# Optimization experiments

Measured on AMD Instinct MI355X. Metric: run time of the kernel, lower is better.

The kernel has to match this reference:

```python
import jax, jax.numpy as jnp
import numpy as np

SIZE = 512
NUM_HEADS = 8
HEAD_SIZE = SIZE // NUM_HEADS
EPS = 1e-5  # GroupNorm default eps


def setup_inputs() -> dict:
    key = jax.random.key(0)
    ks = jax.random.split(key, 8)
    B, T, D = 2, 2048, SIZE
    mk = lambda k: jax.random.normal(k, (D, D), dtype=jnp.float32) / D
    return {
        "x": jax.random.normal(ks[0], (B, T, D), dtype=jnp.float32),
        "W_Q": mk(ks[1]),
        "W_K": mk(ks[2]),
        "W_V": mk(ks[3]),
        "W_G": mk(ks[4]),
        "W_O": mk(ks[5]),
        "gn_weight": jnp.ones((D,), dtype=jnp.float32),
        "gn_bias": jnp.zeros((D,), dtype=jnp.float32),
    }


def _retention(x, W_Q, W_K, W_V):
    B, T, D = x.shape
    H, dh = NUM_HEADS, HEAD_SIZE
    # projections -> (B, H, T, dh)
    q = (x @ W_Q).reshape(B, T, H, dh).transpose(0, 2, 1, 3)
    k = (x @ W_K).reshape(B, T, H, dh).transpose(0, 2, 1, 3)
    v = (x @ W_V).reshape(B, T, H, dh).transpose(0, 2, 1, 3)
    # multi-scale per-head decay: gamma_h = 1 - 2^{-5-h}
    gammas = 1.0 - jnp.exp2(-5.0 - jnp.arange(H, dtype=jnp.float32))
    idx = jnp.arange(T)
    diff = (idx[:, None] - idx[None, :]).astype(jnp.float32)  # (T, T)
    causal = diff >= 0
    # D[h, n, m] = gamma_h^{n-m} for n >= m else 0
    decay = jnp.where(causal[None], jnp.exp(diff[None] * jnp.log(gammas)[:, None, None]), 0.0)
    scores = jnp.einsum("bhtd,bhsd->bhts", q, k) / jnp.sqrt(jnp.float32(dh))
    out = jnp.einsum("bhts,bhsd->bhtd", scores * decay[None], v)
    return out.transpose(0, 2, 1, 3).reshape(B, T, D)


def _group_norm(y, weight, bias):
    # GroupNorm(NUM_HEADS, SIZE) over flattened (B*T, SIZE)
    B, T, D = y.shape
    g = y.reshape(B * T, NUM_HEADS, HEAD_SIZE)
    mean = jnp.mean(g, axis=-1, keepdims=True)
    var = jnp.var(g, axis=-1, keepdims=True)
    g = (g - mean) / jnp.sqrt(var + EPS)
    g = g.reshape(B * T, D) * weight + bias
    return g.reshape(B, T, D)


def reference(x, W_Q, W_K, W_V, W_G, W_O, gn_weight, gn_bias):
    ret = _retention(x, W_Q, W_K, W_V)          # (B, T, D)
    normed = _group_norm(ret, gn_weight, gn_bias)  # (B, T, D)
    return jax.nn.silu(x @ W_G + normed) @ W_O
```

## Files before the change

kernel.cpp:

```cpp
#include <hip/hip_runtime.h>
#include <hip/hip_bf16.h>
#include <math.h>

#define DMODEL 512
#define T_SEQ 2048
#define NH 8
#define DH 64
#define M_ROWS 4096
#define LDST 72
#define EPST 136

typedef short s16x8 __attribute__((ext_vector_type(8)));
typedef float f32x4 __attribute__((ext_vector_type(4)));

static __device__ __forceinline__ unsigned short f2bf(float f) {
  __hip_bfloat16 h = __float2bfloat16(f);
  return *(unsigned short*)&h;
}
static __device__ __forceinline__ float bf2f(unsigned short u) {
  union { unsigned int i; float f; } x; x.i = (unsigned int)u << 16; return x.f;
}
static __device__ __forceinline__ void gld16(void* lds, const void* g) {
  __builtin_amdgcn_global_load_lds(
      (const __attribute__((address_space(1))) unsigned int*)g,
      (__attribute__((address_space(3))) unsigned int*)lds, 16, 0, 0);
}

__global__ __launch_bounds__(256) void prep_k(
    const float* __restrict__ x, unsigned short* __restrict__ Xb,
    const float* __restrict__ W0, const float* __restrict__ W1,
    const float* __restrict__ W2, const float* __restrict__ W3,
    const float* __restrict__ W4, unsigned short* __restrict__ WT)
{
  __shared__ __align__(16) unsigned short buf[64 * LDST];
  const int bid = blockIdx.x, tid = threadIdx.x;
  if (bid < 1024) {
    const size_t i = ((size_t)bid * 256 + tid) * 8;
    float4 a = *(const float4*)&x[i];
    float4 b = *(const float4*)&x[i + 4];
    s16x8 o;
    o[0]=f2bf(a.x); o[1]=f2bf(a.y); o[2]=f2bf(a.z); o[3]=f2bf(a.w);
    o[4]=f2bf(b.x); o[5]=f2bf(b.y); o[6]=f2bf(b.z); o[7]=f2bf(b.w);
    *(s16x8*)&Xb[i] = o;
    return;
  }
  const int bid2 = bid - 1024;
  const int z = bid2 >> 6, rem = bid2 & 63;
  const int n0 = (rem & 7) * 64, k0 = (rem >> 3) * 64;
  const float* W = (z==0)?W0:(z==1)?W1:(z==2)?W2:(z==3)?W3:W4;
  int rowbase;
  if (z == 0)      rowbase = n0;
  else if (z == 1) rowbase = 512 + (n0 >> 6) * 128;
  else if (z == 2) rowbase = 512 + (n0 >> 6) * 128 + 64;
  else if (z == 3) rowbase = 1536 + n0;
  else             rowbase = 2048 + n0;
  #pragma unroll
  for (int r = 0; r < 4; ++r) {
    int idx = r * 256 + tid;
    int kr = idx >> 4, nc = idx & 15;
    float4 v = *(const float4*)&W[(size_t)(k0 + kr) * DMODEL + n0 + nc * 4];
    buf[(nc*4+0) * LDST + kr] = f2bf(v.x);
    buf[(nc*4+1) * LDST + kr] = f2bf(v.y);
    buf[(nc*4+2) * LDST + kr] = f2bf(v.z);
    buf[(nc*4+3) * LDST + kr] = f2bf(v.w);
  }
  __syncthreads();
  #pragma unroll
  for (int r = 0; r < 2; ++r) {
    int idx = r * 256 + tid;
    int nr = idx >> 3, c = idx & 7;
    *(s16x8*)&WT[((size_t)(rowbase + nr)) * DMODEL + k0 + c * 8] =
        *(const s16x8*)&buf[nr * LDST + c * 8];
  }
}

__global__ __launch_bounds__(256) void proj_kv_k(
    const unsigned short* __restrict__ A, const unsigned short* __restrict__ BT,
    unsigned short* __restrict__ Qb, unsigned short* __restrict__ Kb,
    unsigned short* __restrict__ Vb, unsigned short* __restrict__ Gb,
    float* __restrict__ AT)
{
  __shared__ __align__(16) unsigned short smem[128 * EPST];
  unsigned short* As = smem;
  unsigned short* Bs = smem + 128 * 64;
  const int ng0 = blockIdx.x * 128;
  const int m0 = blockIdx.y * 128;
  const int tid = threadIdx.x;
  const int wave = tid >> 6, lane = tid & 63;
  const int wm = wave >> 1, wn = wave & 1;
  const int n = lane & 15, quad = lane >> 4;

  int srow[4], scol[4];
  #pragma unroll
  for (int r = 0; r < 4; ++r) {
    int idx = r * 256 + tid;
    srow[r] = idx >> 3;
    scol[r] = ((idx & 7) ^ (srow[r] & 7)) * 8;
  }

  f32x4 acc[4][4];
  #pragma unroll
  for (int mi = 0; mi < 4; ++mi)
    #pragma unroll
    for (int ni = 0; ni < 4; ++ni) acc[mi][ni] = (f32x4){0.f,0.f,0.f,0.f};

  for (int k0 = 0; k0 < 512; k0 += 64) {
    #pragma unroll
    for (int r = 0; r < 4; ++r) {
      int idx = r * 256 + tid;
      gld16(&As[idx * 8], &A[(size_t)(m0 + srow[r]) * DMODEL + k0 + scol[r]]);
      gld16(&Bs[idx * 8], &BT[(size_t)(ng0 + srow[r]) * DMODEL + k0 + scol[r]]);
    }
    __syncthreads();
    #pragma unroll
    for (int kk = 0; kk < 2; ++kk) {
      s16x8 af[4], bf[4];
      #pragma unroll
      for (int mi = 0; mi < 4; ++mi) {
        int R = wm*64 + mi*16 + n, cc = (kk*4 + quad) ^ (n & 7);
        af[mi] = *(const s16x8*)&As[R * 64 + cc * 8];
      }
      #pragma unroll
      for (int ni = 0; ni < 4; ++ni) {
        int R = wn*64 + ni*16 + n, cc = (kk*4 + quad) ^ (n & 7);
        bf[ni] = *(const s16x8*)&Bs[R * 64 + cc * 8];
      }
      #pragma unroll
      for (int mi = 0; mi < 4; ++mi)
        #pragma unroll
        for (int ni = 0; ni < 4; ++ni)
          acc[mi][ni] = __builtin_amdgcn_mfma_f32_16x16x32_bf16(
              af[mi], bf[ni], acc[mi][ni], 0, 0, 0);
    }
    __syncthreads();
  }

  unsigned short* Ep = smem;
  #pragma unroll
  for (int mi = 0; mi < 4; ++mi)
    #pragma unroll
    for (int ni = 0; ni < 4; ++ni)
      #pragma unroll
      for (int r = 0; r < 4; ++r)
        Ep[(wm*64 + mi*16 + quad*4 + r) * EPST + wn*64 + ni*16 + n] =
            f2bf(acc[mi][ni][r]);
  __syncthreads();

  const int bx = blockIdx.x;
  if (bx < 4 || bx >= 12) {
    unsigned short* Cz = (bx < 4) ? Qb : Gb;
    const int n0 = (bx < 4) ? ng0 : (ng0 - 1536);
    #pragma unroll
    for (int t = 0; t < 8; ++t) {
      int idx = t * 256 + tid;
      int row = idx >> 4, u = idx & 15;
      *(s16x8*)&Cz[(size_t)(m0 + row) * DMODEL + n0 + u * 8] =
          *(const s16x8*)&Ep[row * EPST + u * 8];
    }
    return;
  }

  const int h = (ng0 - 512) >> 7;
  const float lg = log2f(1.0f - exp2f(-5.0f - (float)h));
  #pragma unroll
  for (int t = 0; t < 4; ++t) {
    int idx = t * 256 + tid;
    int row = idx >> 3, u = idx & 7;
    *(s16x8*)&Kb[(size_t)(m0 + row) * DMODEL + h*DH + u * 8] =
        *(const s16x8*)&Ep[row * EPST + u * 8];
    *(s16x8*)&Vb[(size_t)(m0 + row) * DMODEL + h*DH + u * 8] =
        *(const s16x8*)&Ep[row * EPST + 64 + u * 8];
  }

  unsigned short* Kt = smem;
  unsigned short* Vt = smem + 64 * LDST;
  #pragma unroll
  for (int cc2 = 0; cc2 < 2; ++cc2) {
    __syncthreads();
    if (wm == cc2) {
      unsigned short* Tt = (wn == 0) ? Kt : Vt;
      #pragma unroll
      for (int mi = 0; mi < 4; ++mi)
        #pragma unroll
        for (int r = 0; r < 4; ++r) {
          int m = mi*16 + quad*4 + r;
          float sc = (wn == 0) ? exp2f((float)(64 - m) * lg) : 1.0f;
          #pragma unroll
          for (int ni = 0; ni < 4; ++ni)
            Tt[(ni*16 + n) * LDST + m] = f2bf(acc[mi][ni][r] * sc);
        }
    }
    __syncthreads();
    f32x4 at[4];
    #pragma unroll
    for (int j = 0; j < 4; ++j) at[j] = (f32x4){0.f,0.f,0.f,0.f};
    #pragma unroll
    for (int kk = 0; kk < 2; ++kk) {
      s16x8 a = *(const s16x8*)&Vt[(wave*16 + n) * LDST + kk*32 + quad*8];
      #pragma unroll
      for (int j = 0; j < 4; ++j) {
        s16x8 bf = *(const s16x8*)&Kt[(j*16 + n) * LDST + kk*32 + quad*8];
        at[j] = __builtin_amdgcn_mfma_f32_16x16x32_bf16(a, bf, at[j], 0, 0, 0);
      }
    }
    const int gr = m0 + cc2 * 64;
    const int bb = gr >> 11, cchunk = (gr & 2047) >> 6;
    float* Ab = AT + (((size_t)(bb * NH + h) * 32 + cchunk) << 12);
    #pragma unroll
    for (int j = 0; j < 4; ++j)
      #pragma unroll
      for (int r = 0; r < 4; ++r)
        Ab[(wave*16 + quad*4 + r) * 64 + j*16 + n] = at[j][r];
  }
}

__global__ __launch_bounds__(256) void ret_o2_k(
    const unsigned short* __restrict__ Qb, const unsigned short* __restrict__ Kb,
    const unsigned short* __restrict__ Vb, const float* __restrict__ AT,
    const unsigned short* __restrict__ Gg, const float* __restrict__ gnw,
    const float* __restrict__ gnb, unsigned short* __restrict__ Sb)
{
  __shared__ __align__(16) unsigned short Qs[64 * 64];
  __shared__ __align__(16) unsigned short Ks[64 * 64];
  __shared__ __align__(16) unsigned short Vst[64 * LDST];
  __shared__ __align__(16) unsigned short Ss[64 * LDST];
  __shared__ __align__(16) unsigned short Ps[64 * LDST];
  const int c = (int)gridDim.x - 1 - (int)blockIdx.x;
  const int h = blockIdx.y, b = blockIdx.z;
  const int bh = b * NH + h;
  const int tid = threadIdx.x;
  const int wave = tid >> 6, lane = tid & 63;
  const int n = lane & 15, quad = lane >> 4;
  const size_t base = ((size_t)b * T_SEQ + (size_t)c * 64) * DMODEL + h * DH;
  const float lg = log2f(1.0f - exp2f(-5.0f - (float)h));
  const float lg64 = 64.0f * lg;

  #pragma unroll
  for (int r = 0; r < 2; ++r) {
    int idx = r * 256 + tid;
    int row = idx >> 3, sc = ((idx & 7) ^ (row & 7)) * 8;
    gld16(&Qs[idx * 8], &Qb[base + (size_t)row * DMODEL + sc]);
    gld16(&Ks[idx * 8], &Kb[base + (size_t)row * DMODEL + sc]);
  }
  #pragma unroll
  for (int r = 0; r < 2; ++r) {
    int idx = r * 256 + tid;
    int m = idx & 63, ch = idx >> 6;
    s16x8 vv = *(const s16x8*)&Vb[base + (size_t)m * DMODEL + ch * 8];
    #pragma unroll
    for (int e = 0; e < 8; ++e)
      Vst[(ch * 8 + e) * LDST + m] = ((unsigned short*)&vv)[e];
  }

  const float* Ac = AT + (((size_t)bh * 32) << 12) + (size_t)tid * 16;
  float4 S0 = {0,0,0,0}, S1 = S0, S2 = S0, S3 = S0;
  #pragma unroll 4
  for (int cp = 0; cp < c; ++cp) {
    const float* p = Ac + ((size_t)cp << 12);
    const float w = exp2f((float)(c - 1 - cp) * lg64);
    float4 a0 = *(const float4*)(p + 0);
    float4 a1 = *(const float4*)(p + 4);
    float4 a2 = *(const float4*)(p + 8);
    float4 a3 = *(const float4*)(p + 12);
    S0.x = fmaf(w, a0.x, S0.x); S0.y = fmaf(w, a0.y, S0.y);
    S0.z = fmaf(w, a0.z, S0.z); S0.w = fmaf(w, a0.w, S0.w);
    S1.x = fmaf(w, a1.x, S1.x); S1.y = fmaf(w, a1.y, S1.y);
    S1.z = fmaf(w, a1.z, S1.z); S1.w = fmaf(w, a1.w, S1.w);
    S2.x = fmaf(w, a2.x, S2.x); S2.y = fmaf(w, a2.y, S2.y);
    S2.z = fmaf(w, a2.z, S2.z); S2.w = fmaf(w, a2.w, S2.w);
    S3.x = fmaf(w, a3.x, S3.x); S3.y = fmaf(w, a3.y, S3.y);
    S3.z = fmaf(w, a3.z, S3.z); S3.w = fmaf(w, a3.w, S3.w);
  }
  {
    const int d2 = tid >> 2, d1b = (tid & 3) * 16;
    s16x8 lo, hi;
    lo[0]=f2bf(S0.x); lo[1]=f2bf(S0.y); lo[2]=f2bf(S0.z); lo[3]=f2bf(S0.w);
    lo[4]=f2bf(S1.x); lo[5]=f2bf(S1.y); lo[6]=f2bf(S1.z); lo[7]=f2bf(S1.w);
    hi[0]=f2bf(S2.x); hi[1]=f2bf(S2.y); hi[2]=f2bf(S2.z); hi[3]=f2bf(S2.w);
    hi[4]=f2bf(S3.x); hi[5]=f2bf(S3.y); hi[6]=f2bf(S3.z); hi[7]=f2bf(S3.w);
    *(s16x8*)&Ss[d2 * LDST + d1b] = lo;
    *(s16x8*)&Ss[d2 * LDST + d1b + 8] = hi;
  }
  __syncthreads();

  f32x4 s[4], u[4];
  #pragma unroll
  for (int j = 0; j < 4; ++j) {
    s[j] = (f32x4){0.f,0.f,0.f,0.f};
    u[j] = (f32x4){0.f,0.f,0.f,0.f};
  }
  const int RA = wave*16 + n;
  #pragma unroll
  for (int kk = 0; kk < 2; ++kk) {
    s16x8 a = *(const s16x8*)&Qs[RA * 64 + (((kk*4 + quad) ^ (RA & 7)) * 8)];
    #pragma unroll
    for (int j = 0; j < 4; ++j) {
      int RB = j*16 + n;
      s16x8 bk = *(const s16x8*)&Ks[RB * 64 + (((kk*4 + quad) ^ (RB & 7)) * 8)];
      s[j] = __builtin_amdgcn_mfma_f32_16x16x32_bf16(a, bk, s[j], 0, 0, 0);
      s16x8 bs = *(const s16x8*)&Ss[RB * LDST + kk*32 + quad*8];
      u[j] = __builtin_amdgcn_mfma_f32_16x16x32_bf16(a, bs, u[j], 0, 0, 0);
    }
  }

  float rowf[4], colf[4];
  #pragma unroll
  for (int r = 0; r < 4; ++r) rowf[r] = exp2f((float)(wave*16 + quad*4 + r) * lg);
  #pragma unroll
  for (int j = 0; j < 4; ++j) colf[j] = exp2f(-(float)(j*16 + n) * lg);

  #pragma unroll
  for (int j = 0; j < 4; ++j)
    #pragma unroll
    for (int r = 0; r < 4; ++r) {
      int i = wave*16 + quad*4 + r, mcol = j*16 + n;
      float v = (mcol <= i) ? s[j][r] * 0.125f * rowf[r] * colf[j] : 0.0f;
      Ps[i * LDST + mcol] = f2bf(v);
    }
  __syncthreads();

  #pragma unroll
  for (int r = 0; r < 2; ++r) {
    int idx = r * 256 + tid;
    int row = idx >> 3, sc = ((idx & 7) ^ (row & 7)) * 8;
    gld16(&Qs[idx * 8], &Gg[base + (size_t)row * DMODEL + sc]);
  }

  f32x4 acc[4];
  #pragma unroll
  for (int j = 0; j < 4; ++j) acc[j] = (f32x4){0.f,0.f,0.f,0.f};
  #pragma unroll
  for (int kk = 0; kk < 2; ++kk) {
    s16x8 a = *(const s16x8*)&Ps[RA * LDST + kk*32 + quad*8];
    #pragma unroll
    for (int j = 0; j < 4; ++j) {
      s16x8 bf = *(const s16x8*)&Vst[(j*16 + n) * LDST + kk*32 + quad*8];
      acc[j] = __builtin_amdgcn_mfma_f32_16x16x32_bf16(a, bf, acc[j], 0, 0, 0);
    }
  }

  float ov[4][4];
  #pragma unroll
  for (int j = 0; j < 4; ++j)
    #pragma unroll
    for (int r = 0; r < 4; ++r)
      ov[j][r] = acc[j][r] + 0.125f * rowf[r] * u[j][r];

  float gw[4], gb[4];
  #pragma unroll
  for (int j = 0; j < 4; ++j) {
    gw[j] = gnw[h*DH + j*16 + n];
    gb[j] = gnb[h*DH + j*16 + n];
  }

  float normed[4][4];
  #pragma unroll
  for (int r = 0; r < 4; ++r) {
    float sum = ov[0][r] + ov[1][r] + ov[2][r] + ov[3][r];
    float sq  = ov[0][r]*ov[0][r] + ov[1][r]*ov[1][r]
              + ov[2][r]*ov[2][r] + ov[3][r]*ov[3][r];
    #pragma unroll
    for (int off = 8; off > 0; off >>= 1) {
      sum += __shfl_xor(sum, off, 64);
      sq  += __shfl_xor(sq,  off, 64);
    }
    const float mean = sum * (1.0f / 64.0f);
    float var = sq * (1.0f / 64.0f) - mean * mean;
    var = fmaxf(var, 0.0f);
    const float rstd = rsqrtf(var + 1e-5f);
    #pragma unroll
    for (int j = 0; j < 4; ++j)
      normed[j][r] = (ov[j][r] - mean) * rstd * gw[j] + gb[j];
  }

  __syncthreads();

  #pragma unroll
  for (int r = 0; r < 4; ++r) {
    const int i = wave*16 + quad*4 + r;
    #pragma unroll
    for (int j = 0; j < 4; ++j) {
      const int col = j*16 + n;
      const int gidx = i * 64 + (((col >> 3) ^ (i & 7)) * 8) + (col & 7);
      float uu = bf2f(Qs[gidx]) + normed[j][r];
      Ps[i * LDST + col] = f2bf(uu / (1.0f + expf(-uu)));
    }
  }
  __syncthreads();
  #pragma unroll
  for (int t = 0; t < 2; ++t) {
    int idx = t * 256 + tid;
    int row = idx >> 3, u8 = idx & 7;
    *(s16x8*)&Sb[base + (size_t)row * DMODEL + u8 * 8] =
        *(const s16x8*)&Ps[row * LDST + u8 * 8];
  }
}

__global__ __launch_bounds__(256) void out_gemm_k(
    const unsigned short* __restrict__ A, const unsigned short* __restrict__ BT,
    float* __restrict__ out)
{
  __shared__ __align__(16) unsigned short As[64 * 64];
  __shared__ __align__(16) unsigned short Bs[64 * 64];
  const int n0 = blockIdx.x * 64;
  const int m0 = blockIdx.y * 64;
  const int tid = threadIdx.x;
  const int wave = tid >> 6, lane = tid & 63;
  const int wm = wave >> 1, wn = wave & 1;
  const int n = lane & 15, quad = lane >> 4;

  int srow[2], scol[2];
  #pragma unroll
  for (int r = 0; r < 2; ++r) {
    int idx = r * 256 + tid;
    srow[r] = idx >> 3;
    scol[r] = ((idx & 7) ^ (srow[r] & 7)) * 8;
  }

  f32x4 acc[2][2];
  #pragma unroll
  for (int mi = 0; mi < 2; ++mi)
    #pragma unroll
    for (int ni = 0; ni < 2; ++ni) acc[mi][ni] = (f32x4){0.f,0.f,0.f,0.f};

  for (int k0 = 0; k0 < 512; k0 += 64) {
    #pragma unroll
    for (int r = 0; r < 2; ++r) {
      int idx = r * 256 + tid;
      gld16(&As[idx * 8], &A[(size_t)(m0 + srow[r]) * DMODEL + k0 + scol[r]]);
      gld16(&Bs[idx * 8], &BT[(size_t)(n0 + srow[r]) * DMODEL + k0 + scol[r]]);
    }
    __syncthreads();
    #pragma unroll
    for (int kk = 0; kk < 2; ++kk) {
      s16x8 af[2], bf[2];
      #pragma unroll
      for (int mi = 0; mi < 2; ++mi) {
        int R = wm*32 + mi*16 + n, cc = (kk*4 + quad) ^ (n & 7);
        af[mi] = *(const s16x8*)&As[R * 64 + cc * 8];
      }
      #pragma unroll
      for (int ni = 0; ni < 2; ++ni) {
        int R = wn*32 + ni*16 + n, cc = (kk*4 + quad) ^ (n & 7);
        bf[ni] = *(const s16x8*)&Bs[R * 64 + cc * 8];
      }
      #pragma unroll
      for (int mi = 0; mi < 2; ++mi)
        #pragma unroll
        for (int ni = 0; ni < 2; ++ni)
          acc[mi][ni] = __builtin_amdgcn_mfma_f32_16x16x32_bf16(
              af[mi], bf[ni], acc[mi][ni], 0, 0, 0);
    }
    __syncthreads();
  }

  #pragma unroll
  for (int mi = 0; mi < 2; ++mi)
    #pragma unroll
    for (int ni = 0; ni < 2; ++ni)
      #pragma unroll
      for (int r = 0; r < 4; ++r)
        out[(size_t)(m0 + wm*32 + mi*16 + quad*4 + r) * DMODEL +
            n0 + wn*32 + ni*16 + n] = acc[mi][ni][r];
}

extern "C" void kernel_launch(void* const* d_in, const int* in_sizes, int n_in,
                              void* d_out, int out_size, void* d_ws, size_t ws_size,
                              hipStream_t stream) {
  const float* x   = (const float*)d_in[0];
  const float* WQ  = (const float*)d_in[1];
  const float* WK  = (const float*)d_in[2];
  const float* WV  = (const float*)d_in[3];
  const float* WG  = (const float*)d_in[4];
  const float* WO  = (const float*)d_in[5];
  const float* gnw = (const float*)d_in[6];
  const float* gnb = (const float*)d_in[7];
  float* out = (float*)d_out;

  char* ws = (char*)d_ws;
  unsigned short* Xb = (unsigned short*)(ws);
  unsigned short* Qb = (unsigned short*)(ws + 4  * (1<<20));
  unsigned short* Kb = (unsigned short*)(ws + 8  * (1<<20));
  unsigned short* Vb = (unsigned short*)(ws + 12 * (1<<20));
  unsigned short* G  = (unsigned short*)(ws + 16 * (1<<20));
  float* AT  = (float*)(ws + 24 * (1<<20));
  unsigned short* Sb = (unsigned short*)(ws + 32 * (1<<20));
  unsigned short* WT = (unsigned short*)(ws + 40 * (1<<20));
  (void)ws_size;

  prep_k<<<dim3(1024 + 320), 256, 0, stream>>>(x, Xb, WQ, WK, WV, WG, WO, WT);
  proj_kv_k<<<dim3(16, M_ROWS / 128), 256, 0, stream>>>(
      Xb, WT, Qb, Kb, Vb, G, AT);
  ret_o2_k<<<dim3(T_SEQ / 64, NH, 2), 256, 0, stream>>>(
      Qb, Kb, Vb, AT, G, gnw, gnb, Sb);
  out_gemm_k<<<dim3(8, M_ROWS / 64), 256, 0, stream>>>(
      Sb, WT + 2048 * DMODEL, out);
}
```

Baseline: 122.4 us.

## Fuse four kernels into one persistent kernel with grid-wide barriers

Replaces the four separate launches (prep, projection, retention, output GEMM) with a single persistent kernel of 512 blocks. The stages are separated by software grid barriers built on atomic counters in workspace, which is reset with a memset before launch. This removes per-launch overhead and the idle gaps between kernels. In exchange it adds barrier spin cost, fixes the shared-memory size to the largest stage, and relies on all 512 blocks being co-resident (launch bounds of 2 blocks per CU), otherwise the barrier can deadlock.

```diff
diff --git a/kernel.cpp b/kernel.cpp
--- a/kernel.cpp
+++ b/kernel.cpp
@@ -9,6 +9,7 @@
 #define M_ROWS 4096
 #define LDST 72
 #define EPST 136
+#define NBLK 512u
 
 typedef short s16x8 __attribute__((ext_vector_type(8)));
 typedef float f32x4 __attribute__((ext_vector_type(4)));
@@ -26,473 +27,473 @@
       (__attribute__((address_space(3))) unsigned int*)lds, 16, 0, 0);
 }
 
-__global__ __launch_bounds__(256) void prep_k(
-    const float* __restrict__ x, unsigned short* __restrict__ Xb,
-    const float* __restrict__ W0, const float* __restrict__ W1,
-    const float* __restrict__ W2, const float* __restrict__ W3,
-    const float* __restrict__ W4, unsigned short* __restrict__ WT)
-{
-  __shared__ __align__(16) unsigned short buf[64 * LDST];
-  const int bid = blockIdx.x, tid = threadIdx.x;
-  if (bid < 1024) {
-    const size_t i = ((size_t)bid * 256 + tid) * 8;
-    float4 a = *(const float4*)&x[i];
-    float4 b = *(const float4*)&x[i + 4];
-    s16x8 o;
-    o[0]=f2bf(a.x); o[1]=f2bf(a.y); o[2]=f2bf(a.z); o[3]=f2bf(a.w);
-    o[4]=f2bf(b.x); o[5]=f2bf(b.y); o[6]=f2bf(b.z); o[7]=f2bf(b.w);
-    *(s16x8*)&Xb[i] = o;
-    return;
-  }
-  const int bid2 = bid - 1024;
-  const int z = bid2 >> 6, rem = bid2 & 63;
-  const int n0 = (rem & 7) * 64, k0 = (rem >> 3) * 64;
-  const float* W = (z==0)?W0:(z==1)?W1:(z==2)?W2:(z==3)?W3:W4;
-  int rowbase;
-  if (z == 0)      rowbase = n0;
-  else if (z == 1) rowbase = 512 + (n0 >> 6) * 128;
-  else if (z == 2) rowbase = 512 + (n0 >> 6) * 128 + 64;
-  else if (z == 3) rowbase = 1536 + n0;
-  else             rowbase = 2048 + n0;
-  #pragma unroll
-  for (int r = 0; r < 4; ++r) {
-    int idx = r * 256 + tid;
-    int kr = idx >> 4, nc = idx & 15;
-    float4 v = *(const float4*)&W[(size_t)(k0 + kr) * DMODEL + n0 + nc * 4];
-    buf[(nc*4+0) * LDST + kr] = f2bf(v.x);
-    buf[(nc*4+1) * LDST + kr] = f2bf(v.y);
-    buf[(nc*4+2) * LDST + kr] = f2bf(v.z);
-    buf[(nc*4+3) * LDST + kr] = f2bf(v.w);
+static __device__ __forceinline__ void gbar(unsigned int* cnt) {
+  __syncthreads();
+  if (threadIdx.x == 0) {
+    __threadfence();
+    __hip_atomic_fetch_add(cnt, 1u, __ATOMIC_RELEASE, __HIP_MEMORY_SCOPE_AGENT);
+    while (__hip_atomic_load(cnt, __ATOMIC_ACQUIRE, __HIP_MEMORY_SCOPE_AGENT)
+           < NBLK) {
+      __builtin_amdgcn_s_sleep(2);
+    }
   }
   __syncthreads();
-  #pragma unroll
-  for (int r = 0; r < 2; ++r) {
-    int idx = r * 256 + tid;
-    int nr = idx >> 3, c = idx & 7;
-    *(s16x8*)&WT[((size_t)(rowbase + nr)) * DMODEL + k0 + c * 8] =
-        *(const s16x8*)&buf[nr * LDST + c * 8];
+}
+
+struct MegaArgs {
+  const float* x;
+  const float* W0; const float* W1; const float* W2;
+  const float* W3; const float* W4;
+  const float* gnw; const float* gnb;
+  unsigned short* Xb; unsigned short* WT;
+  unsigned short* Qb; unsigned short* Kb; unsigned short* Vb;
+  unsigned short* G;  unsigned short* Sb;
+  float* AT; float* out;
+  unsigned int* bar;
+};
+
+__global__ __launch_bounds__(256, 2) void mega_k(MegaArgs a)
+{
+  __shared__ __align__(16) unsigned short smem[22016];
+  const int bid = blockIdx.x, tid = threadIdx.x;
+  const int wave = tid >> 6, lane = tid & 63;
+  const int n = lane & 15, quad = lane >> 4;
+
+  for (int u = bid; u < 1344; u += 512) {
+    if (u < 1024) {
+      const size_t i = ((size_t)u * 256 + tid) * 8;
+      float4 av = *(const float4*)&a.x[i];
+      float4 bv = *(const float4*)&a.x[i + 4];
+      s16x8 o;
+      o[0]=f2bf(av.x); o[1]=f2bf(av.y); o[2]=f2bf(av.z); o[3]=f2bf(av.w);
+      o[4]=f2bf(bv.x); o[5]=f2bf(bv.y); o[6]=f2bf(bv.z); o[7]=f2bf(bv.w);
+      *(s16x8*)&a.Xb[i] = o;
+    } else {
+      const int bid2 = u - 1024;
+      const int z = bid2 >> 6, rem = bid2 & 63;
+      const int n0 = (rem & 7) * 64, k0 = (rem >> 3) * 64;
+      const float* W = (z==0)?a.W0:(z==1)?a.W1:(z==2)?a.W2:(z==3)?a.W3:a.W4;
+      int rowbase;
+      if (z == 0)      rowbase = n0;
+      else if (z == 1) rowbase = 512 + (n0 >> 6) * 128;
+      else if (z == 2) rowbase = 512 + (n0 >> 6) * 128 + 64;
+      else if (z == 3) rowbase = 1536 + n0;
+      else             rowbase = 2048 + n0;
+      unsigned short* buf = smem;
+      #pragma unroll
+      for (int r = 0; r < 4; ++r) {
+        int idx = r * 256 + tid;
+        int kr = idx >> 4, nc = idx & 15;
+        float4 v = *(const float4*)&W[(size_t)(k0 + kr) * DMODEL + n0 + nc * 4];
+        buf[(nc*4+0) * LDST + kr] = f2bf(v.x);
+        buf[(nc*4+1) * LDST + kr] = f2bf(v.y);
+        buf[(nc*4+2) * LDST + kr] = f2bf(v.z);
+        buf[(nc*4+3) * LDST + kr] = f2bf(v.w);
+      }
+      __syncthreads();
+      #pragma unroll
+      for (int r = 0; r < 2; ++r) {
+        int idx = r * 256 + tid;
+        int nr = idx >> 3, c8 = idx & 7;
+        *(s16x8*)&a.WT[((size_t)(rowbase + nr)) * DMODEL + k0 + c8 * 8] =
+            *(const s16x8*)&buf[nr * LDST + c8 * 8];
+      }
+      __syncthreads();
+    }
   }
-}
-
-__global__ __launch_bounds__(256) void proj_kv_k(
-    const unsigned short* __restrict__ A, const unsigned short* __restrict__ BT,
-    unsigned short* __restrict__ Qb, unsigned short* __restrict__ Kb,
-    unsigned short* __restrict__ Vb, unsigned short* __restrict__ Gb,
-    float* __restrict__ AT)
-{
-  __shared__ __align__(16) unsigned short smem[128 * EPST];
-  unsigned short* As = smem;
-  unsigned short* Bs = smem + 128 * 64;
-  const int ng0 = blockIdx.x * 128;
-  const int m0 = blockIdx.y * 128;
-  const int tid = threadIdx.x;
-  const int wave = tid >> 6, lane = tid & 63;
-  const int wm = wave >> 1, wn = wave & 1;
-  const int n = lane & 15, quad = lane >> 4;
-
-  int srow[4], scol[4];
-  #pragma unroll
-  for (int r = 0; r < 4; ++r) {
-    int idx = r * 256 + tid;
-    srow[r] = idx >> 3;
-    scol[r] = ((idx & 7) ^ (srow[r] & 7)) * 8;
-  }
-
-  f32x4 acc[4][4];
-  #pragma unroll
-  for (int mi = 0; mi < 4; ++mi)
-    #pragma unroll
-    for (int ni = 0; ni < 4; ++ni) acc[mi][ni] = (f32x4){0.f,0.f,0.f,0.f};
-
-  for (int k0 = 0; k0 < 512; k0 += 64) {
+  gbar(&a.bar[0]);
+
+  {
+    unsigned short* As = smem;
+    unsigned short* Bs = smem + 128 * 64;
+    const int bx = bid & 15, by = bid >> 4;
+    const int ng0 = bx * 128, m0 = by * 128;
+    const int wm = wave >> 1, wn = wave & 1;
+
+    int srow[4], scol[4];
     #pragma unroll
     for (int r = 0; r < 4; ++r) {
       int idx = r * 256 + tid;
-      gld16(&As[idx * 8], &A[(size_t)(m0 + srow[r]) * DMODEL + k0 + scol[r]]);
-      gld16(&Bs[idx * 8], &BT[(size_t)(ng0 + srow[r]) * DMODEL + k0 + scol[r]]);
-    }
-    __syncthreads();
-    #pragma unroll
-    for (int kk = 0; kk < 2; ++kk) {
-      s16x8 af[4], bf[4];
-      #pragma unroll
-      for (int mi = 0; mi < 4; ++mi) {
-        int R = wm*64 + mi*16 + n, cc = (kk*4 + quad) ^ (n & 7);
-        af[mi] = *(const s16x8*)&As[R * 64 + cc * 8];
-      }
-      #pragma unroll
-      for (int ni = 0; ni < 4; ++ni) {
-        int R = wn*64 + ni*16 + n, cc = (kk*4 + quad) ^ (n & 7);
-        bf[ni] = *(const s16x8*)&Bs[R * 64 + cc * 8];
-      }
-      #pragma unroll
-      for (int mi = 0; mi < 4; ++mi)
-        #pragma unroll
-        for (int ni = 0; ni < 4; ++ni)
-          acc[mi][ni] = __builtin_amdgcn_mfma_f32_16x16x32_bf16(
-              af[mi], bf[ni], acc[mi][ni], 0, 0, 0);
-    }
-    __syncthreads();
-  }
-
-  unsigned short* Ep = smem;
-  #pragma unroll
-  for (int mi = 0; mi < 4; ++mi)
-    #pragma unroll
-    for (int ni = 0; ni < 4; ++ni)
-      #pragma unroll
-      for (int r = 0; r < 4; ++r)
-        Ep[(wm*64 + mi*16 + quad*4 + r) * EPST + wn*64 + ni*16 + n] =
-            f2bf(acc[mi][ni][r]);
-  __syncthreads();
-
-  const int bx = blockIdx.x;
-  if (bx < 4 || bx >= 12) {
-    unsigned short* Cz = (bx < 4) ? Qb : Gb;
-    const int n0 = (bx < 4) ? ng0 : (ng0 - 1536);
-    #pragma unroll
-    for (int t = 0; t < 8; ++t) {
-      int idx = t * 256 + tid;
-      int row = idx >> 4, u = idx & 15;
-      *(s16x8*)&Cz[(size_t)(m0 + row) * DMODEL + n0 + u * 8] =
-          *(const s16x8*)&Ep[row * EPST + u * 8];
-    }
-    return;
-  }
-
-  const int h = (ng0 - 512) >> 7;
-  const float lg = log2f(1.0f - exp2f(-5.0f - (float)h));
-  #pragma unroll
-  for (int t = 0; t < 4; ++t) {
-    int idx = t * 256 + tid;
-    int row = idx >> 3, u = idx & 7;
-    *(s16x8*)&Kb[(size_t)(m0 + row) * DMODEL + h*DH + u * 8] =
-        *(const s16x8*)&Ep[row * EPST + u * 8];
-    *(s16x8*)&Vb[(size_t)(m0 + row) * DMODEL + h*DH + u * 8] =
-        *(const s16x8*)&Ep[row * EPST + 64 + u * 8];
-  }
-
-  unsigned short* Kt = smem;
-  unsigned short* Vt = smem + 64 * LDST;
-  #pragma unroll
-  for (int cc2 = 0; cc2 < 2; ++cc2) {
-    __syncthreads();
-    if (wm == cc2) {
-      unsigned short* Tt = (wn == 0) ? Kt : Vt;
-      #pragma unroll
-      for (int mi = 0; mi < 4; ++mi)
-        #pragma unroll
-        for (int r = 0; r < 4; ++r) {
-          int m = mi*16 + quad*4 + r;
-          float sc = (wn == 0) ? exp2f((float)(64 - m) * lg) : 1.0f;
+      srow[r] = idx >> 3;
+      scol[r] = ((idx & 7) ^ (srow[r] & 7)) * 8;
+    }
+
+    f32x4 acc[4][4];
+    #pragma unroll
+    for (int mi = 0; mi < 4; ++mi)
+      #pragma unroll
+      for (int ni = 0; ni < 4; ++ni) acc[mi][ni] = (f32x4){0.f,0.f,0.f,0.f};
+
+    for (int k0 = 0; k0 < 512; k0 += 64) {
+      #pragma unroll
+      for (int r = 0; r < 4; ++r) {
+        int idx = r * 256 + tid;
+        gld16(&As[idx * 8], &a.Xb[(size_t)(m0 + srow[r]) * DMODEL + k0 + scol[r]]);
+        gld16(&Bs[idx * 8], &a.WT[(size_t)(ng0 + srow[r]) * DMODEL + k0 + scol[r]]);
+      }
+      __syncthreads();
+      #pragma unroll
+      for (int kk = 0; kk < 2; ++kk) {
+        s16x8 af[4], bf[4];
+        #pragma unroll
+        for (int mi = 0; mi < 4; ++mi) {
+          int R = wm*64 + mi*16 + n, cc = (kk*4 + quad) ^ (n & 7);
+          af[mi] = *(const s16x8*)&As[R * 64 + cc * 8];
+        }
+        #pragma unroll
+        for (int ni = 0; ni < 4; ++ni) {
+          int R = wn*64 + ni*16 + n, cc = (kk*4 + quad) ^ (n & 7);
+          bf[ni] = *(const s16x8*)&Bs[R * 64 + cc * 8];
+        }
+        #pragma unroll
+        for (int mi = 0; mi < 4; ++mi)
           #pragma unroll
           for (int ni = 0; ni < 4; ++ni)
-            Tt[(ni*16 + n) * LDST + m] = f2bf(acc[mi][ni][r] * sc);
-        }
-    }
+            acc[mi][ni] = __builtin_amdgcn_mfma_f32_16x16x32_bf16(
+                af[mi], bf[ni], acc[mi][ni], 0, 0, 0);
+      }
+      __syncthreads();
+    }
+
+    unsigned short* Ep = smem;
+    #pragma unroll
+    for (int mi = 0; mi < 4; ++mi)
+      #pragma unroll
+      for (int ni = 0; ni < 4; ++ni)
+        #pragma unroll
+        for (int r = 0; r < 4; ++r)
+          Ep[(wm*64 + mi*16 + quad*4 + r) * EPST + wn*64 + ni*16 + n] =
+              f2bf(acc[mi][ni][r]);
     __syncthreads();
-    f32x4 at[4];
-    #pragma unroll
-    for (int j = 0; j < 4; ++j) at[j] = (f32x4){0.f,0.f,0.f,0.f};
-    #pragma unroll
-    for (int kk = 0; kk < 2; ++kk) {
-      s16x8 a = *(const s16x8*)&Vt[(wave*16 + n) * LDST + kk*32 + quad*8];
-      #pragma unroll
-      for (int j = 0; j < 4; ++j) {
-        s16x8 bf = *(const s16x8*)&Kt[(j*16 + n) * LDST + kk*32 + quad*8];
-        at[j] = __builtin_amdgcn_mfma_f32_16x16x32_bf16(a, bf, at[j], 0, 0, 0);
-      }
-    }
-    const int gr = m0 + cc2 * 64;
-    const int bb = gr >> 11, cchunk = (gr & 2047) >> 6;
-    float* Ab = AT + (((size_t)(bb * NH + h) * 32 + cchunk) << 12);
-    #pragma unroll
-    for (int j = 0; j < 4; ++j)
-      #pragma unroll
-      for (int r = 0; r < 4; ++r)
-        Ab[(wave*16 + quad*4 + r) * 64 + j*16 + n] = at[j][r];
+
+    if (bx < 4 || bx >= 12) {
+      unsigned short* Cz = (bx < 4) ? a.Qb : a.G;
+      const int n0 = (bx < 4) ? ng0 : (ng0 - 1536);
+      #pragma unroll
+      for (int t = 0; t < 8; ++t) {
+        int idx = t * 256 + tid;
+        int row = idx >> 4, u = idx & 15;
+        *(s16x8*)&Cz[(size_t)(m0 + row) * DMODEL + n0 + u * 8] =
+            *(const s16x8*)&Ep[row * EPST + u * 8];
+      }
+    } else {
+      const int h = (ng0 - 512) >> 7;
+      const float lg = log2f(1.0f - exp2f(-5.0f - (float)h));
+      #pragma unroll
+      for (int t = 0; t < 4; ++t) {
+        int idx = t * 256 + tid;
+        int row = idx >> 3, u = idx & 7;
+        *(s16x8*)&a.Kb[(size_t)(m0 + row) * DMODEL + h*DH + u * 8] =
+            *(const s16x8*)&Ep[row * EPST + u * 8];
+        *(s16x8*)&a.Vb[(size_t)(m0 + row) * DMODEL + h*DH + u * 8] =
+            *(const s16x8*)&Ep[row * EPST + 64 + u * 8];
+      }
+      unsigned short* Kt = smem;
+      unsigned short* Vt = smem + 64 * LDST;
+      #pragma unroll
+      for (int cc2 = 0; cc2 < 2; ++cc2) {
+        __syncthreads();
+        if (wm == cc2) {
+          unsigned short* Tt = (wn == 0) ? Kt : Vt;
+          #pragma unroll
+          for (int mi = 0; mi < 4; ++mi)
+            #pragma unroll
+            for (int r = 0; r < 4; ++r) {
+              int m = mi*16 + quad*4 + r;
+              float sc = (wn == 0) ? exp2f((float)(64 - m) * lg) : 1.0f;
+              #pragma unroll
+              for (int ni = 0; ni < 4; ++ni)
+                Tt[(ni*16 + n) * LDST + m] = f2bf(acc[mi][ni][r] * sc);
+            }
+        }
+        __syncthreads();
+        f32x4 at[4];
+        #pragma unroll
+        for (int j = 0; j < 4; ++j) at[j] = (f32x4){0.f,0.f,0.f,0.f};
+        #pragma unroll
+        for (int kk = 0; kk < 2; ++kk) {
+          s16x8 av = *(const s16x8*)&Vt[(wave*16 + n) * LDST + kk*32 + quad*8];
+          #pragma unroll
+          for (int j = 0; j < 4; ++j) {
+            s16x8 bf = *(const s16x8*)&Kt[(j*16 + n) * LDST + kk*32 + quad*8];
+            at[j] = __builtin_amdgcn_mfma_f32_16x16x32_bf16(av, bf, at[j], 0, 0, 0);
+          }
+        }
+        const int gr = m0 + cc2 * 64;
+        const int bb = gr >> 11, cchunk = (gr & 2047) >> 6;
+        float* Ab = a.AT + (((size_t)(bb * NH + h) * 32 + cchunk) << 12);
+        #pragma unroll
+        for (int j = 0; j < 4; ++j)
+          #pragma unroll
+          for (int r = 0; r < 4; ++r)
+            Ab[(wave*16 + quad*4 + r) * 64 + j*16 + n] = at[j][r];
+      }
+    }
   }
-}
-
-__global__ __launch_bounds__(256) void ret_o2_k(
-    const unsigned short* __restrict__ Qb, const unsigned short* __restrict__ Kb,
-    const unsigned short* __restrict__ Vb, const float* __restrict__ AT,
-    const unsigned short* __restrict__ Gg, const float* __restrict__ gnw,
-    const float* __restrict__ gnb, unsigned short* __restrict__ Sb)
-{
-  __shared__ __align__(16) unsigned short Qs[64 * 64];
-  __shared__ __align__(16) unsigned short Ks[64 * 64];
-  __shared__ __align__(16) unsigned short Vst[64 * LDST];
-  __shared__ __align__(16) unsigned short Ss[64 * LDST];
-  __shared__ __align__(16) unsigned short Ps[64 * LDST];
-  const int c = (int)gridDim.x - 1 - (int)blockIdx.x;
-  const int h = blockIdx.y, b = blockIdx.z;
-  const int bh = b * NH + h;
-  const int tid = threadIdx.x;
-  const int wave = tid >> 6, lane = tid & 63;
-  const int n = lane & 15, quad = lane >> 4;
-  const size_t base = ((size_t)b * T_SEQ + (size_t)c * 64) * DMODEL + h * DH;
-  const float lg = log2f(1.0f - exp2f(-5.0f - (float)h));
-  const float lg64 = 64.0f * lg;
-
-  #pragma unroll
-  for (int r = 0; r < 2; ++r) {
-    int idx = r * 256 + tid;
-    int row = idx >> 3, sc = ((idx & 7) ^ (row & 7)) * 8;
-    gld16(&Qs[idx * 8], &Qb[base + (size_t)row * DMODEL + sc]);
-    gld16(&Ks[idx * 8], &Kb[base + (size_t)row * DMODEL + sc]);
-  }
-  #pragma unroll
-  for (int r = 0; r < 2; ++r) {
-    int idx = r * 256 + tid;
-    int m = idx & 63, ch = idx >> 6;
-    s16x8 vv = *(const s16x8*)&Vb[base + (size_t)m * DMODEL + ch * 8];
-    #pragma unroll
-    for (int e = 0; e < 8; ++e)
-      Vst[(ch * 8 + e) * LDST + m] = ((unsigned short*)&vv)[e];
-  }
-
-  const float* Ac = AT + (((size_t)bh * 32) << 12) + (size_t)tid * 16;
-  float4 S0 = {0,0,0,0}, S1 = S0, S2 = S0, S3 = S0;
-  #pragma unroll 4
-  for (int cp = 0; cp < c; ++cp) {
-    const float* p = Ac + ((size_t)cp << 12);
-    const float w = exp2f((float)(c - 1 - cp) * lg64);
-    float4 a0 = *(const float4*)(p + 0);
-    float4 a1 = *(const float4*)(p + 4);
-    float4 a2 = *(const float4*)(p + 8);
-    float4 a3 = *(const float4*)(p + 12);
-    S0.x = fmaf(w, a0.x, S0.x); S0.y = fmaf(w, a0.y, S0.y);
-    S0.z = fmaf(w, a0.z, S0.z); S0.w = fmaf(w, a0.w, S0.w);
-    S1.x = fmaf(w, a1.x, S1.x); S1.y = fmaf(w, a1.y, S1.y);
-    S1.z = fmaf(w, a1.z, S1.z); S1.w = fmaf(w, a1.w, S1.w);
-    S2.x = fmaf(w, a2.x, S2.x); S2.y = fmaf(w, a2.y, S2.y);
-    S2.z = fmaf(w, a2.z, S2.z); S2.w = fmaf(w, a2.w, S2.w);
-    S3.x = fmaf(w, a3.x, S3.x); S3.y = fmaf(w, a3.y, S3.y);
-    S3.z = fmaf(w, a3.z, S3.z); S3.w = fmaf(w, a3.w, S3.w);
-  }
+  gbar(&a.bar[16]);
+
   {
-    const int d2 = tid >> 2, d1b = (tid & 3) * 16;
-    s16x8 lo, hi;
-    lo[0]=f2bf(S0.x); lo[1]=f2bf(S0.y); lo[2]=f2bf(S0.z); lo[3]=f2bf(S0.w);
-    lo[4]=f2bf(S1.x); lo[5]=f2bf(S1.y); lo[6]=f2bf(S1.z); lo[7]=f2bf(S1.w);
-    hi[0]=f2bf(S2.x); hi[1]=f2bf(S2.y); hi[2]=f2bf(S2.z); hi[3]=f2bf(S2.w);
-    hi[4]=f2bf(S3.x); hi[5]=f2bf(S3.y); hi[6]=f2bf(S3.z); hi[7]=f2bf(S3.w);
-    *(s16x8*)&Ss[d2 * LDST + d1b] = lo;
-    *(s16x8*)&Ss[d2 * LDST + d1b + 8] = hi;
-  }
-  __syncthreads();
-
-  f32x4 s[4], u[4];
-  #pragma unroll
-  for (int j = 0; j < 4; ++j) {
-    s[j] = (f32x4){0.f,0.f,0.f,0.f};
-    u[j] = (f32x4){0.f,0.f,0.f,0.f};
-  }
-  const int RA = wave*16 + n;
-  #pragma unroll
-  for (int kk = 0; kk < 2; ++kk) {
-    s16x8 a = *(const s16x8*)&Qs[RA * 64 + (((kk*4 + quad) ^ (RA & 7)) * 8)];
-    #pragma unroll
-    for (int j = 0; j < 4; ++j) {
-      int RB = j*16 + n;
-      s16x8 bk = *(const s16x8*)&Ks[RB * 64 + (((kk*4 + quad) ^ (RB & 7)) * 8)];
-      s[j] = __builtin_amdgcn_mfma_f32_16x16x32_bf16(a, bk, s[j], 0, 0, 0);
-      s16x8 bs = *(const s16x8*)&Ss[RB * LDST + kk*32 + quad*8];
-      u[j] = __builtin_amdgcn_mfma_f32_16x16x32_bf16(a, bs, u[j], 0, 0, 0);
-    }
-  }
-
-  float rowf[4], colf[4];
-  #pragma unroll
-  for (int r = 0; r < 4; ++r) rowf[r] = exp2f((float)(wave*16 + quad*4 + r) * lg);
-  #pragma unroll
-  for (int j = 0; j < 4; ++j) colf[j] = exp2f(-(float)(j*16 + n) * lg);
-
-  #pragma unroll
-  for (int j = 0; j < 4; ++j)
-    #pragma unroll
-    for (int r = 0; r < 4; ++r) {
-      int i = wave*16 + quad*4 + r, mcol = j*16 + n;
-      float v = (mcol <= i) ? s[j][r] * 0.125f * rowf[r] * colf[j] : 0.0f;
-      Ps[i * LDST + mcol] = f2bf(v);
-    }
-  __syncthreads();
-
-  #pragma unroll
-  for (int r = 0; r < 2; ++r) {
-    int idx = r * 256 + tid;
-    int row = idx >> 3, sc = ((idx & 7) ^ (row & 7)) * 8;
-    gld16(&Qs[idx * 8], &Gg[base + (size_t)row * DMODEL + sc]);
-  }
-
-  f32x4 acc[4];
-  #pragma unroll
-  for (int j = 0; j < 4; ++j) acc[j] = (f32x4){0.f,0.f,0.f,0.f};
-  #pragma unroll
-  for (int kk = 0; kk < 2; ++kk) {
-    s16x8 a = *(const s16x8*)&Ps[RA * LDST + kk*32 + quad*8];
-    #pragma unroll
-    for (int j = 0; j < 4; ++j) {
-      s16x8 bf = *(const s16x8*)&Vst[(j*16 + n) * LDST + kk*32 + quad*8];
-      acc[j] = __builtin_amdgcn_mfma_f32_16x16x32_bf16(a, bf, acc[j], 0, 0, 0);
-    }
-  }
-
-  float ov[4][4];
-  #pragma unroll
-  for (int j = 0; j < 4; ++j)
-    #pragma unroll
-    for (int r = 0; r < 4; ++r)
-      ov[j][r] = acc[j][r] + 0.125f * rowf[r] * u[j][r];
-
-  float gw[4], gb[4];
-  #pragma unroll
-  for (int j = 0; j < 4; ++j) {
-    gw[j] = gnw[h*DH + j*16 + n];
-    gb[j] = gnb[h*DH + j*16 + n];
-  }
-
-  float normed[4][4];
-  #pragma unroll
-  for (int r = 0; r < 4; ++r) {
-    float sum = ov[0][r] + ov[1][r] + ov[2][r] + ov[3][r];
-    float sq  = ov[0][r]*ov[0][r] + ov[1][r]*ov[1][r]
-              + ov[2][r]*ov[2][r] + ov[3][r]*ov[3][r];
-    #pragma unroll
-    for (int off = 8; off > 0; off >>= 1) {
-      sum += __shfl_xor(sum, off, 64);
-      sq  += __shfl_xor(sq,  off, 64);
-    }
-    const float mean = sum * (1.0f / 64.0f);
-    float var = sq * (1.0f / 64.0f) - mean * mean;
-    var = fmaxf(var, 0.0f);
-    const float rstd = rsqrtf(var + 1e-5f);
-    #pragma unroll
-    for (int j = 0; j < 4; ++j)
-      normed[j][r] = (ov[j][r] - mean) * rstd * gw[j] + gb[j];
-  }
-
-  __syncthreads();
-
-  #pragma unroll
-  for (int r = 0; r < 4; ++r) {
-    const int i = wave*16 + quad*4 + r;
-    #pragma unroll
-    for (int j = 0; j < 4; ++j) {
-      const int col = j*16 + n;
-      const int gidx = i * 64 + (((col >> 3) ^ (i & 7)) * 8) + (col & 7);
-      float uu = bf2f(Qs[gidx]) + normed[j][r];
-      Ps[i * LDST + col] = f2bf(uu / (1.0f + expf(-uu)));
-    }
-  }
-  __syncthreads();
-  #pragma unroll
-  for (int t = 0; t < 2; ++t) {
-    int idx = t * 256 + tid;
-    int row = idx >> 3, u8 = idx & 7;
-    *(s16x8*)&Sb[base + (size_t)row * DMODEL + u8 * 8] =
-        *(const s16x8*)&Ps[row * LDST + u8 * 8];
-  }
-}
-
-__global__ __launch_bounds__(256) void out_gemm_k(
-    const unsigned short* __restrict__ A, const unsigned short* __restrict__ BT,
-    float* __restrict__ out)
-{
-  __shared__ __align__(16) unsigned short As[64 * 64];
-  __shared__ __align__(16) unsigned short Bs[64 * 64];
-  const int n0 = blockIdx.x * 64;
-  const int m0 = blockIdx.y * 64;
-  const int tid = threadIdx.x;
-  const int wave = tid >> 6, lane = tid & 63;
-  const int wm = wave >> 1, wn = wave & 1;
-  const int n = lane & 15, quad = lane >> 4;
-
-  int srow[2], scol[2];
-  #pragma unroll
-  for (int r = 0; r < 2; ++r) {
-    int idx = r * 256 + tid;
-    srow[r] = idx >> 3;
-    scol[r] = ((idx & 7) ^ (srow[r] & 7)) * 8;
-  }
-
-  f32x4 acc[2][2];
-  #pragma unroll
-  for (int mi = 0; mi < 2; ++mi)
-    #pragma unroll
-    for (int ni = 0; ni < 2; ++ni) acc[mi][ni] = (f32x4){0.f,0.f,0.f,0.f};
-
-  for (int k0 = 0; k0 < 512; k0 += 64) {
+    unsigned short* Qs  = smem;
+    unsigned short* Ks  = smem + 4096;
+    unsigned short* Vst = smem + 8192;
+    unsigned short* Ss  = smem + 8192 + 4608;
+    unsigned short* Ps  = smem + 8192 + 9216;
+    const int c = bid & 31, h = (bid >> 5) & 7, b = bid >> 8;
+    const int bh = b * NH + h;
+    const size_t base = ((size_t)b * T_SEQ + (size_t)c * 64) * DMODEL + h * DH;
+    const float lg = log2f(1.0f - exp2f(-5.0f - (float)h));
+    const float lg64 = 64.0f * lg;
+
     #pragma unroll
     for (int r = 0; r < 2; ++r) {
       int idx = r * 256 + tid;
-      gld16(&As[idx * 8], &A[(size_t)(m0 + srow[r]) * DMODEL + k0 + scol[r]]);
-      gld16(&Bs[idx * 8], &BT[(size_t)(n0 + srow[r]) * DMODEL + k0 + scol[r]]);
+      int row = idx >> 3, sc = ((idx & 7) ^ (row & 7)) * 8;
+      gld16(&Qs[idx * 8], &a.Qb[base + (size_t)row * DMODEL + sc]);
+      gld16(&Ks[idx * 8], &a.Kb[base + (size_t)row * DMODEL + sc]);
+    }
+    #pragma unroll
+    for (int r = 0; r < 2; ++r) {
+      int idx = r * 256 + tid;
+      int m = idx & 63, ch = idx >> 6;
+      s16x8 vv = *(const s16x8*)&a.Vb[base + (size_t)m * DMODEL + ch * 8];
+      #pragma unroll
+      for (int e = 0; e < 8; ++e)
+        Vst[(ch * 8 + e) * LDST + m] = ((unsigned short*)&vv)[e];
+    }
+
+    const float* Ac = a.AT + (((size_t)bh * 32) << 12) + (size_t)tid * 16;
+    float4 S0 = {0,0,0,0}, S1 = S0, S2 = S0, S3 = S0;
+    #pragma unroll 4
+    for (int cp = 0; cp < c; ++cp) {
+      const float* p = Ac + ((size_t)cp << 12);
+      const float w = exp2f((float)(c - 1 - cp) * lg64);
+      float4 a0 = *(const float4*)(p + 0);
+      float4 a1 = *(const float4*)(p + 4);
+      float4 a2 = *(const float4*)(p + 8);
+      float4 a3 = *(const float4*)(p + 12);
+      S0.x = fmaf(w, a0.x, S0.x); S0.y = fmaf(w, a0.y, S0.y);
+      S0.z = fmaf(w, a0.z, S0.z); S0.w = fmaf(w, a0.w, S0.w);
+      S1.x = fmaf(w, a1.x, S1.x); S1.y = fmaf(w, a1.y, S1.y);
+      S1.z = fmaf(w, a1.z, S1.z); S1.w = fmaf(w, a1.w, S1.w);
+      S2.x = fmaf(w, a2.x, S2.x); S2.y = fmaf(w, a2.y, S2.y);
+      S2.z = fmaf(w, a2.z, S2.z); S2.w = fmaf(w, a2.w, S2.w);
+      S3.x = fmaf(w, a3.x, S3.x); S3.y = fmaf(w, a3.y, S3.y);
+      S3.z = fmaf(w, a3.z, S3.z); S3.w = fmaf(w, a3.w, S3.w);
+    }
+    {
+      const int d2 = tid >> 2, d1b = (tid & 3) * 16;
+      s16x8 lo, hi;
+      lo[0]=f2bf(S0.x); lo[1]=f2bf(S0.y); lo[2]=f2bf(S0.z); lo[3]=f2bf(S0.w);
+      lo[4]=f2bf(S1.x); lo[5]=f2bf(S1.y); lo[6]=f2bf(S1.z); lo[7]=f2bf(S1.w);
+      hi[0]=f2bf(S2.x); hi[1]=f2bf(S2.y); hi[2]=f2bf(S2.z); hi[3]=f2bf(S2.w);
+      hi[4]=f2bf(S3.x); hi[5]=f2bf(S3.y); hi[6]=f2bf(S3.z); hi[7]=f2bf(S3.w);
+      *(s16x8*)&Ss[d2 * LDST + d1b] = lo;
+      *(s16x8*)&Ss[d2 * LDST + d1b + 8] = hi;
     }
     __syncthreads();
+
+    f32x4 s[4], u[4];
+    #pragma unroll
+    for (int j = 0; j < 4; ++j) {
+      s[j] = (f32x4){0.f,0.f,0.f,0.f};
+      u[j] = (f32x4){0.f,0.f,0.f,0.f};
+    }
+    const int RA = wave*16 + n;
     #pragma unroll
     for (int kk = 0; kk < 2; ++kk) {
-      s16x8 af[2], bf[2];
-      #pragma unroll
-      for (int mi = 0; mi < 2; ++mi) {
-        int R = wm*32 + mi*16 + n, cc = (kk*4 + quad) ^ (n & 7);
-        af[mi] = *(const s16x8*)&As[R * 64 + cc * 8];
-      }
-      #pragma unroll
-      for (int ni = 0; ni < 2; ++ni) {
-        int R = wn*32 + ni*16 + n, cc = (kk*4 + quad) ^ (n & 7);
-        bf[ni] = *(const s16x8*)&Bs[R * 64 + cc * 8];
-      }
-      #pragma unroll
-      for (int mi = 0; mi < 2; ++mi)
-        #pragma unroll
-        for (int ni = 0; ni < 2; ++ni)
-          acc[mi][ni] = __builtin_amdgcn_mfma_f32_16x16x32_bf16(
-              af[mi], bf[ni], acc[mi][ni], 0, 0, 0);
-    }
+      s16x8 av = *(const s16x8*)&Qs[RA * 64 + (((kk*4 + quad) ^ (RA & 7)) * 8)];
+      #pragma unroll
+      for (int j = 0; j < 4; ++j) {
+        int RB = j*16 + n;
+        s16x8 bk = *(const s16x8*)&Ks[RB * 64 + (((kk*4 + quad) ^ (RB & 7)) * 8)];
+        s[j] = __builtin_amdgcn_mfma_f32_16x16x32_bf16(av, bk, s[j], 0, 0, 0);
+        s16x8 bs = *(const s16x8*)&Ss[RB * LDST + kk*32 + quad*8];
+        u[j] = __builtin_amdgcn_mfma_f32_16x16x32_bf16(av, bs, u[j], 0, 0, 0);
+      }
+    }
+
+    float rowf[4], colf[4];
+    #pragma unroll
+    for (int r = 0; r < 4; ++r) rowf[r] = exp2f((float)(wave*16 + quad*4 + r) * lg);
+    #pragma unroll
+    for (int j = 0; j < 4; ++j) colf[j] = exp2f(-(float)(j*16 + n) * lg);
+
+    #pragma unroll
+    for (int j = 0; j < 4; ++j)
+      #pragma unroll
+      for (int r = 0; r < 4; ++r) {
+        int i = wave*16 + quad*4 + r, mcol = j*16 + n;
+        float v = (mcol <= i) ? s[j][r] * 0.125f * rowf[r] * colf[j] : 0.0f;
+        Ps[i * LDST + mcol] = f2bf(v);
+      }
     __syncthreads();
+
+    #pragma unroll
+    for (int r = 0; r < 2; ++r) {
+      int idx = r * 256 + tid;
+      int row = idx >> 3, sc = ((idx & 7) ^ (row & 7)) * 8;
+      gld16(&Qs[idx * 8], &a.G[base + (size_t)row * DMODEL + sc]);
+    }
+
+    f32x4 acc[4];
+    #pragma unroll
+    for (int j = 0; j < 4; ++j) acc[j] = (f32x4){0.f,0.f,0.f,0.f};
+    #pragma unroll
+    for (int kk = 0; kk < 2; ++kk) {
+      s16x8 av = *(const s16x8*)&Ps[RA * LDST + kk*32 + quad*8];
+      #pragma unroll
+      for (int j = 0; j < 4; ++j) {
+        s16x8 bf = *(const s16x8*)&Vst[(j*16 + n) * LDST + kk*32 + quad*8];
+        acc[j] = __builtin_amdgcn_mfma_f32_16x16x32_bf16(av, bf, acc[j], 0, 0, 0);
+      }
+    }
+
+    float ov[4][4];
+    #pragma unroll
+    for (int j = 0; j < 4; ++j)
+      #pragma unroll
+      for (int r = 0; r < 4; ++r)
+        ov[j][r] = acc[j][r] + 0.125f * rowf[r] * u[j][r];
+
+    float gw[4], gb[4];
+    #pragma unroll
+    for (int j = 0; j < 4; ++j) {
+      gw[j] = a.gnw[h*DH + j*16 + n];
+      gb[j] = a.gnb[h*DH + j*16 + n];
+    }
+
+    float normed[4][4];
+    #pragma unroll
+    for (int r = 0; r < 4; ++r) {
+      float sum = ov[0][r] + ov[1][r] + ov[2][r] + ov[3][r];
+      float sq  = ov[0][r]*ov[0][r] + ov[1][r]*ov[1][r]
+                + ov[2][r]*ov[2][r] + ov[3][r]*ov[3][r];
+      #pragma unroll
+      for (int off = 8; off > 0; off >>= 1) {
+        sum += __shfl_xor(sum, off, 64);
+        sq  += __shfl_xor(sq,  off, 64);
+      }
+      const float mean = sum * (1.0f / 64.0f);
+      float var = sq * (1.0f / 64.0f) - mean * mean;
+      var = fmaxf(var, 0.0f);
+      const float rstd = rsqrtf(var + 1e-5f);
+      #pragma unroll
+      for (int j = 0; j < 4; ++j)
+        normed[j][r] = (ov[j][r] - mean) * rstd * gw[j] + gb[j];
+    }
+
+    __syncthreads();
+
+    #pragma unroll
+    for (int r = 0; r < 4; ++r) {
+      const int i = wave*16 + quad*4 + r;
+      #pragma unroll
+      for (int j = 0; j < 4; ++j) {
+        const int col = j*16 + n;
+        const int gidx = i * 64 + (((col >> 3) ^ (i & 7)) * 8) + (col & 7);
+        float uu = bf2f(Qs[gidx]) + normed[j][r];
+        Ps[i * LDST + col] = f2bf(uu / (1.0f + expf(-uu)));
+      }
+    }
+    __syncthreads();
+    #pragma unroll
+    for (int t = 0; t < 2; ++t) {
+      int idx = t * 256 + tid;
+      int row = idx >> 3, u8 = idx & 7;
+      *(s16x8*)&a.Sb[base + (size_t)row * DMODEL + u8 * 8] =
+          *(const s16x8*)&Ps[row * LDST + u8 * 8];
+    }
   }
-
-  #pragma unroll
-  for (int mi = 0; mi < 2; ++mi)
-    #pragma unroll
-    for (int ni = 0; ni < 2; ++ni)
-      #pragma unroll
-      for (int r = 0; r < 4; ++r)
-        out[(size_t)(m0 + wm*32 + mi*16 + quad*4 + r) * DMODEL +
-            n0 + wn*32 + ni*16 + n] = acc[mi][ni][r];
+  gbar(&a.bar[32]);
+
+  {
+    unsigned short* As = smem;
+    unsigned short* Bs = smem + 4096;
+    const unsigned short* BT = a.WT + 2048 * DMODEL;
+    const int n0 = (bid & 7) * 64, m0 = (bid >> 3) * 64;
+    const int wm = wave >> 1, wn = wave & 1;
+
+    int srow[2], scol[2];
+    #pragma unroll
+    for (int r = 0; r < 2; ++r) {
+      int idx = r * 256 + tid;
+      srow[r] = idx >> 3;
+      scol[r] = ((idx & 7) ^ (srow[r] & 7)) * 8;
+    }
+
+    f32x4 acc[2][2];
+    #pragma unroll
+    for (int mi = 0; mi < 2; ++mi)
+      #pragma unroll
+      for (int ni = 0; ni < 2; ++ni) acc[mi][ni] = (f32x4){0.f,0.f,0.f,0.f};
+
+    for (int k0 = 0; k0 < 512; k0 += 64) {
+      #pragma unroll
+      for (int r = 0; r < 2; ++r) {
+        int idx = r * 256 + tid;
+        gld16(&As[idx * 8], &a.Sb[(size_t)(m0 + srow[r]) * DMODEL + k0 + scol[r]]);
+        gld16(&Bs[idx * 8], &BT[(size_t)(n0 + srow[r]) * DMODEL + k0 + scol[r]]);
+      }
+      __syncthreads();
+      #pragma unroll
+      for (int kk = 0; kk < 2; ++kk) {
+        s16x8 af[2], bf[2];
+        #pragma unroll
+        for (int mi = 0; mi < 2; ++mi) {
+          int R = wm*32 + mi*16 + n, cc = (kk*4 + quad) ^ (n & 7);
+          af[mi] = *(const s16x8*)&As[R * 64 + cc * 8];
+        }
+        #pragma unroll
+        for (int ni = 0; ni < 2; ++ni) {
+          int R = wn*32 + ni*16 + n, cc = (kk*4 + quad) ^ (n & 7);
+          bf[ni] = *(const s16x8*)&Bs[R * 64 + cc * 8];
+        }
+        #pragma unroll
+        for (int mi = 0; mi < 2; ++mi)
+          #pragma unroll
+          for (int ni = 0; ni < 2; ++ni)
+            acc[mi][ni] = __builtin_amdgcn_mfma_f32_16x16x32_bf16(
+                af[mi], bf[ni], acc[mi][ni], 0, 0, 0);
+      }
+      __syncthreads();
+    }
+
+    #pragma unroll
+    for (int mi = 0; mi < 2; ++mi)
+      #pragma unroll
+      for (int ni = 0; ni < 2; ++ni)
+        #pragma unroll
+        for (int r = 0; r < 4; ++r)
+          a.out[(size_t)(m0 + wm*32 + mi*16 + quad*4 + r) * DMODEL +
+                n0 + wn*32 + ni*16 + n] = acc[mi][ni][r];
+  }
 }
 
 extern "C" void kernel_launch(void* const* d_in, const int* in_sizes, int n_in,
                               void* d_out, int out_size, void* d_ws, size_t ws_size,
                               hipStream_t stream) {
-  const float* x   = (const float*)d_in[0];
-  const float* WQ  = (const float*)d_in[1];
-  const float* WK  = (const float*)d_in[2];
-  const float* WV  = (const float*)d_in[3];
-  const float* WG  = (const float*)d_in[4];
-  const float* WO  = (const float*)d_in[5];
-  const float* gnw = (const float*)d_in[6];
-  const float* gnb = (const float*)d_in[7];
-  float* out = (float*)d_out;
-
   char* ws = (char*)d_ws;
-  unsigned short* Xb = (unsigned short*)(ws);
-  unsigned short* Qb = (unsigned short*)(ws + 4  * (1<<20));
-  unsigned short* Kb = (unsigned short*)(ws + 8  * (1<<20));
-  unsigned short* Vb = (unsigned short*)(ws + 12 * (1<<20));
-  unsigned short* G  = (unsigned short*)(ws + 16 * (1<<20));
-  float* AT  = (float*)(ws + 24 * (1<<20));
-  unsigned short* Sb = (unsigned short*)(ws + 32 * (1<<20));
-  unsigned short* WT = (unsigned short*)(ws + 40 * (1<<20));
+  MegaArgs a;
+  a.x   = (const float*)d_in[0];
+  a.W0  = (const float*)d_in[1];
+  a.W1  = (const float*)d_in[2];
+  a.W2  = (const float*)d_in[3];
+  a.W3  = (const float*)d_in[4];
+  a.W4  = (const float*)d_in[5];
+  a.gnw = (const float*)d_in[6];
+  a.gnb = (const float*)d_in[7];
+  a.Xb  = (unsigned short*)(ws);
+  a.Qb  = (unsigned short*)(ws + 4  * (1<<20));
+  a.Kb  = (unsigned short*)(ws + 8  * (1<<20));
+  a.Vb  = (unsigned short*)(ws + 12 * (1<<20));
+  a.G   = (unsigned short*)(ws + 16 * (1<<20));
+  a.AT  = (float*)(ws + 24 * (1<<20));
+  a.Sb  = (unsigned short*)(ws + 32 * (1<<20));
+  a.WT  = (unsigned short*)(ws + 40 * (1<<20));
+  a.bar = (unsigned int*)(ws + 48 * (1<<20));
+  a.out = (float*)d_out;
   (void)ws_size;
 
-  prep_k<<<dim3(1024 + 320), 256, 0, stream>>>(x, Xb, WQ, WK, WV, WG, WO, WT);
-  proj_kv_k<<<dim3(16, M_ROWS / 128), 256, 0, stream>>>(
-      Xb, WT, Qb, Kb, Vb, G, AT);
-  ret_o2_k<<<dim3(T_SEQ / 64, NH, 2), 256, 0, stream>>>(
-      Qb, Kb, Vb, AT, G, gnw, gnb, Sb);
-  out_gemm_k<<<dim3(8, M_ROWS / 64), 256, 0, stream>>>(
-      Sb, WT + 2048 * DMODEL, out);
-}
+  hipMemsetAsync(a.bar, 0, 256, stream);
+  mega_k<<<dim3(512), dim3(256), 0, stream>>>(a);
+}
```

New measurement: 388.0 us. +216.9%, slower.
